# Kernel tuning notes

Measured on AMD Instinct MI355X. Metric: run time of the kernel, lower is better.

Reference implementation:

```python
import jax, jax.numpy as jnp
import numpy as np

D_MODEL = 1024
H = 16
D_K = D_MODEL // H


def setup_inputs() -> dict:
    key = jax.random.key(0)
    ks = jax.random.split(key, 9)
    s = 0.02
    x = jax.random.normal(ks[0], (2, 2048, D_MODEL), dtype=jnp.float32)
    Wq = jax.random.normal(ks[1], (D_MODEL, D_MODEL), dtype=jnp.float32) * s
    bq = jax.random.normal(ks[2], (D_MODEL,), dtype=jnp.float32) * s
    Wk = jax.random.normal(ks[3], (D_MODEL, D_MODEL), dtype=jnp.float32) * s
    bk = jax.random.normal(ks[4], (D_MODEL,), dtype=jnp.float32) * s
    Wv = jax.random.normal(ks[5], (D_MODEL, D_MODEL), dtype=jnp.float32) * s
    bv = jax.random.normal(ks[6], (D_MODEL,), dtype=jnp.float32) * s
    Wo = jax.random.normal(ks[7], (D_MODEL, D_MODEL), dtype=jnp.float32) * s
    bo = jax.random.normal(ks[8], (D_MODEL,), dtype=jnp.float32) * s
    return {"x": x, "Wq": Wq, "bq": bq, "Wk": Wk, "bk": bk,
            "Wv": Wv, "bv": bv, "Wo": Wo, "bo": bo}


def reference(x, Wq, bq, Wk, bk, Wv, bv, Wo, bo):
    b, s, _ = x.shape
    scale = 1.0 / jnp.sqrt(jnp.float32(D_K))
    # projections; [b, s, d] -> [b, h, s, d_k]
    def split_heads(t):
        return t.reshape(b, s, H, D_K).transpose(0, 2, 1, 3)
    q = split_heads(x @ Wq + bq)
    k = split_heads(x @ Wk + bk)
    v = split_heads(x @ Wv + bv)
    scores = jnp.einsum('bhqd,bhkd->bhqk', q, k) * scale  # [b,h,s,s]
    attn = jax.nn.softmax(scores, axis=-1)
    ctx = jnp.einsum('bhqk,bhkd->bhqd', attn, v)
    ctx = ctx.transpose(0, 2, 1, 3).reshape(b, s, D_MODEL)
    return ctx @ Wo + bo + x
```

## Files before the change

kernel.cpp:

```cpp
#include <hip/hip_runtime.h>
#include <hip/hip_bf16.h>
#include <stdint.h>

#define D_MODEL 1024
#define NH 16
#define DK 64
#define S_LEN 2048

typedef __attribute__((ext_vector_type(8))) __bf16 bf16x8;
typedef __attribute__((ext_vector_type(4))) float f32x4;

#define GLOBAL_AS __attribute__((address_space(1)))
#define LDS_AS    __attribute__((address_space(3)))

__device__ __forceinline__ void async16(const ushort* g, ushort* l) {
    __builtin_amdgcn_global_load_lds(
        (const GLOBAL_AS uint32_t*)(uintptr_t)(const void*)g,
        (LDS_AS uint32_t*)(uint32_t)(uintptr_t)(void*)l,
        16, 0, 0);
}

template <int N>
__device__ __forceinline__ void pipe_barrier() {
    asm volatile("s_waitcnt vmcnt(%0)\n\ts_barrier" :: "n"(N) : "memory");
}

__device__ __forceinline__ float fast_exp2(float x) {
    float r;
    asm("v_exp_f32 %0, %1" : "=v"(r) : "v"(x));
    return r;
}

__device__ __forceinline__ ushort f2bf(float f) {
    union { float f; uint32_t u; } v; v.f = f;
    uint32_t lsb = (v.u >> 16) & 1u;
    return (ushort)((v.u + 0x7fffu + lsb) >> 16);
}

__device__ __forceinline__ uint32_t packbf(float a, float b) {
    union { float f; uint32_t u; } x, y; x.f = a; y.f = b;
    return ((x.u + 0x8000u) >> 16) | ((y.u + 0x8000u) & 0xffff0000u);
}

__device__ __forceinline__ bf16x8 ldfrag(const ushort* p) {
    union { uint4 u; bf16x8 b; } cv;
    cv.u = *(const uint4*)p;
    return cv.b;
}


__global__ void cvt_x_kernel(const float* __restrict__ x, ushort* __restrict__ xb) {
    int i = blockIdx.x * 256 + threadIdx.x;
    float4 v = ((const float4*)x)[i];
    ushort4 o;
    o.x = f2bf(v.x); o.y = f2bf(v.y); o.z = f2bf(v.z); o.w = f2bf(v.w);
    ((ushort4*)xb)[i] = o;
}

__global__ void transpose_cvt4_kernel(
    const float* __restrict__ W0, const float* __restrict__ W1,
    const float* __restrict__ W2, const float* __restrict__ W3,
    ushort* __restrict__ D0, ushort* __restrict__ D1,
    ushort* __restrict__ D2, ushort* __restrict__ D3) {
    const float* W; ushort* D;
    switch (blockIdx.z) {
        case 0: W = W0; D = D0; break;
        case 1: W = W1; D = D1; break;
        case 2: W = W2; D = D2; break;
        default: W = W3; D = D3; break;
    }
    __shared__ float tile[32][33];
    int bx = blockIdx.x * 32, by = blockIdx.y * 32;
    int tx = threadIdx.x, ty = threadIdx.y;
#pragma unroll
    for (int j = 0; j < 32; j += 8)
        tile[ty + j][tx] = W[(size_t)(by + ty + j) * D_MODEL + bx + tx];
    __syncthreads();
#pragma unroll
    for (int j = 0; j < 32; j += 8)
        D[(size_t)(bx + ty + j) * D_MODEL + by + tx] = f2bf(tile[tx][ty + j]);
}

__global__ void cvt_bias_kernel(const float* __restrict__ bq, const float* __restrict__ bk,
                                const float* __restrict__ bv, float* __restrict__ out) {
    int i = blockIdx.x * 256 + threadIdx.x;
    float v = (i < 1024) ? bq[i] : (i < 2048 ? bk[i - 1024] : bv[i - 2048]);
    out[i] = v;
}

template <int MODE>
__global__ __launch_bounds__(256) void gemm_kernel(
    const ushort* __restrict__ A, const ushort* __restrict__ Bt,
    const float* __restrict__ bias,
    ushort* __restrict__ outQ, ushort* __restrict__ outK, ushort* __restrict__ outVt,
    const float* __restrict__ xres, float* __restrict__ outF) {
    constexpr int BN = (MODE == 0) ? 128 : 64;
    constexpr int NI = (MODE == 0) ? 4 : 2;
    constexpr int NS = (MODE == 0) ? 4 : 3;
    __shared__ __align__(16) ushort sA[3][128 * 32];
    __shared__ __align__(16) ushort sB[3][BN * 32];
    const int tid = threadIdx.x;
    const int wave = tid >> 6, lane = tid & 63;
    const int lr = lane & 15, lq = lane >> 4;
    const int srow = lane >> 2;
    const int sc = (lane & 3) ^ ((lane >> 4) & 3);

    const int bid = blockIdx.x;
    const int xcd = bid & 7, lb = bid >> 3;
    int bx, by;
    if (MODE == 0) { bx = xcd * 3 + (lb % 3); by = lb / 3; }
    else           { by = xcd * 4 + (lb & 3); bx = lb >> 2; }
    const int blockM = by * 128;
    const int blockN = bx * BN;
    const int waveM = (wave >> 1) * 64;
    const int waveN = (MODE == 0) ? (wave & 1) * 64 : (wave & 1) * 32;

    auto stage = [&](int k0, ushort* a, ushort* b) {
#pragma unroll
        for (int t = 0; t < 2; t++) {
            int row = wave * 32 + t * 16 + srow;
            async16(&A[(size_t)(blockM + row) * D_MODEL + k0 + sc * 8],
                    &a[(wave * 32 + t * 16) * 32]);
        }
        if (MODE == 0) {
#pragma unroll
            for (int t = 0; t < 2; t++) {
                int row = wave * 32 + t * 16 + srow;
                async16(&Bt[(size_t)(blockN + row) * D_MODEL + k0 + sc * 8],
                        &b[(wave * 32 + t * 16) * 32]);
            }
        } else {
            int row = wave * 16 + srow;
            async16(&Bt[(size_t)(blockN + row) * D_MODEL + k0 + sc * 8],
                    &b[wave * 16 * 32]);
        }
    };

    f32x4 acc[4][NI] = {};
    const int swz = (lq ^ ((lr >> 2) & 3)) * 8;

    stage(0, sA[0], sB[0]);
    stage(32, sA[1], sB[1]);
    __syncthreads();

    int cur = 0;
#pragma unroll 4
    for (int k = 0; k < 32; k++) {
        int nx = cur + 2; if (nx >= 3) nx -= 3;
        if (k + 2 < 32) stage((k + 2) * 32, sA[nx], sB[nx]);
        const ushort* a = sA[cur];
        const ushort* b = sB[cur];
        bf16x8 af[4], bfr[NI];
#pragma unroll
        for (int mi = 0; mi < 4; mi++)
            af[mi] = ldfrag(&a[(waveM + mi * 16 + lr) * 32 + swz]);
#pragma unroll
        for (int ni = 0; ni < NI; ni++)
            bfr[ni] = ldfrag(&b[(waveN + ni * 16 + lr) * 32 + swz]);
#pragma unroll
        for (int mi = 0; mi < 4; mi++)
#pragma unroll
            for (int ni = 0; ni < NI; ni++)
                acc[mi][ni] = __builtin_amdgcn_mfma_f32_16x16x32_bf16(
                    af[mi], bfr[ni], acc[mi][ni], 0, 0, 0);
        if (k < 30) pipe_barrier<NS>();
        else if (k == 30) pipe_barrier<0>();
        cur = (cur == 2) ? 0 : cur + 1;
    }

#pragma unroll
    for (int mi = 0; mi < 4; mi++) {
#pragma unroll
        for (int ni = 0; ni < NI; ni++) {
#pragma unroll
            for (int r = 0; r < 4; r++) {
                int m = blockM + waveM + mi * 16 + lq * 4 + r;
                int n = blockN + waveN + ni * 16 + lr;
                float v = acc[mi][ni][r] + bias[n];
                if (MODE == 0) {
                    int which = n >> 10, c = n & 1023;
                    int h = c >> 6, d = c & 63;
                    int b2 = m >> 11, s = m & 2047;
                    size_t bh = (size_t)(b2 * NH + h);
                    if (which == 0)
                        outQ[(bh * S_LEN + s) * DK + d] = f2bf(v * 0.1803368801f);
                    else if (which == 1)
                        outK[(bh * S_LEN + s) * DK + d] = f2bf(v);
                    else
                        outVt[(bh * DK + d) * S_LEN + s] = f2bf(v);
                } else {
                    size_t idx = (size_t)m * D_MODEL + n;
                    outF[idx] = v + xres[idx];
                }
            }
        }
    }
}

__global__ __launch_bounds__(256, 2) void attn_kernel(
    const ushort* __restrict__ Q, const ushort* __restrict__ Km,
    const ushort* __restrict__ Vt, ushort* __restrict__ ctx) {
    const int bid = blockIdx.x;
    const int xcd = bid & 7, lb = bid >> 3;
    const int bh = xcd * 4 + (lb & 3);
    const int qt = lb >> 2;
    const int q0 = qt * 128;
    __shared__ __align__(16) ushort sK[3][64 * 64];
    __shared__ __align__(16) ushort sV[3][64 * 64];
    __shared__ __align__(16) ushort sQP[4][32 * 64];
    const int tid = threadIdx.x;
    const int wave = tid >> 6, lane = tid & 63;
    const int lr = lane & 15, lq = lane >> 4;
    const int srow = lane >> 3, sp = lane & 7;
    const ushort* Qh = Q + (size_t)bh * S_LEN * DK;
    const ushort* Kh = Km + (size_t)bh * S_LEN * DK;
    const ushort* Vh = Vt + (size_t)bh * DK * S_LEN;
    ushort* sPw = sQP[wave];

#pragma unroll
    for (int t = 0; t < 4; t++) {
        int row = t * 8 + srow;
        int c = sp ^ (row & 7);
        async16(&Qh[(size_t)(q0 + wave * 32 + row) * DK + c * 8],
                &sPw[t * 8 * 64]);
    }

    auto stageKV = [&](int k0, int buf) {
#pragma unroll
        for (int t = 0; t < 2; t++) {
            int row = wave * 16 + t * 8 + srow;
            int c = sp ^ (row & 7);
            async16(&Kh[(size_t)(k0 + row) * DK + c * 8],
                    &sK[buf][(wave * 16 + t * 8) * 64]);
            async16(&Vh[(size_t)row * S_LEN + k0 + c * 8],
                    &sV[buf][(wave * 16 + t * 8) * 64]);
        }
    };

    stageKV(0, 0);
    stageKV(64, 1);
    __syncthreads();

    bf16x8 qf[2][2];
#pragma unroll
    for (int nj = 0; nj < 2; nj++)
#pragma unroll
        for (int kk = 0; kk < 2; kk++)
            qf[nj][kk] = ldfrag(&sPw[(nj * 16 + lr) * 64 +
                                     (((kk * 4 + lq) ^ (lr & 7)) * 8)]);

    union { uint4 u; bf16x8 b; } one_u;
    one_u.u = make_uint4(0x3F803F80u, 0x3F803F80u, 0x3F803F80u, 0x3F803F80u);
    const bf16x8 ones = one_u.b;

    f32x4 cacc[2][4] = {};
    f32x4 ssum[2] = {};

    int cur = 0;
    for (int k = 0; k < 32; k++) {
        int nx = cur + 2; if (nx >= 3) nx -= 3;
        if (k + 2 < 32) stageKV((k + 2) * 64, nx);
        const ushort* sk = sK[cur];
        const ushort* sv = sV[cur];

        f32x4 sacc[4][2] = {};
#pragma unroll
        for (int kk = 0; kk < 2; kk++) {
            bf16x8 kf[4];
            int swz = ((kk * 4 + lq) ^ (lr & 7)) * 8;
#pragma unroll
            for (int mi = 0; mi < 4; mi++)
                kf[mi] = ldfrag(&sk[(mi * 16 + lr) * 64 + swz]);
#pragma unroll
            for (int mi = 0; mi < 4; mi++)
#pragma unroll
                for (int nj = 0; nj < 2; nj++)
                    sacc[mi][nj] = __builtin_amdgcn_mfma_f32_16x16x32_bf16(
                        kf[mi], qf[nj][kk], sacc[mi][nj], 0, 0, 0);
        }

#pragma unroll
        for (int mi = 0; mi < 4; mi++)
#pragma unroll
            for (int nj = 0; nj < 2; nj++) {
                float p0 = fast_exp2(sacc[mi][nj][0]);
                float p1 = fast_exp2(sacc[mi][nj][1]);
                float p2 = fast_exp2(sacc[mi][nj][2]);
                float p3 = fast_exp2(sacc[mi][nj][3]);
                uint2 w;
                w.x = packbf(p0, p1);
                w.y = packbf(p2, p3);
                int physc = (mi * 2 + (lq >> 1)) ^ (lr & 7);
                *(uint2*)&sPw[(nj * 16 + lr) * 64 + physc * 8 + (lq & 1) * 4] = w;
            }

#pragma unroll
        for (int ks = 0; ks < 2; ks++) {
            bf16x8 pf[2], vf[4];
            int swz = ((ks * 4 + lq) ^ (lr & 7)) * 8;
#pragma unroll
            for (int nj = 0; nj < 2; nj++)
                pf[nj] = ldfrag(&sPw[(nj * 16 + lr) * 64 + swz]);
#pragma unroll
            for (int nd = 0; nd < 4; nd++)
                vf[nd] = ldfrag(&sv[(nd * 16 + lr) * 64 + swz]);
#pragma unroll
            for (int nj = 0; nj < 2; nj++)
#pragma unroll
                for (int nd = 0; nd < 4; nd++)
                    cacc[nj][nd] = __builtin_amdgcn_mfma_f32_16x16x32_bf16(
                        pf[nj], vf[nd], cacc[nj][nd], 0, 0, 0);
#pragma unroll
            for (int nj = 0; nj < 2; nj++)
                ssum[nj] = __builtin_amdgcn_mfma_f32_16x16x32_bf16(
                    pf[nj], ones, ssum[nj], 0, 0, 0);
        }

        if (k < 30) pipe_barrier<4>();
        else if (k == 30) pipe_barrier<0>();
        cur = (cur == 2) ? 0 : cur + 1;
    }

    const int b = bh >> 4, h = bh & 15;
    float inv[2][4];
#pragma unroll
    for (int nj = 0; nj < 2; nj++)
#pragma unroll
        for (int r = 0; r < 4; r++)
            inv[nj][r] = __builtin_amdgcn_rcpf(ssum[nj][r]);
#pragma unroll
    for (int nj = 0; nj < 2; nj++)
#pragma unroll
        for (int nd = 0; nd < 4; nd++)
#pragma unroll
            for (int r = 0; r < 4; r++) {
                int qrow = q0 + wave * 32 + nj * 16 + lq * 4 + r;
                int d = nd * 16 + lr;
                float v = cacc[nj][nd][r] * inv[nj][r];
                ctx[(size_t)(b * S_LEN + qrow) * D_MODEL + h * DK + d] = f2bf(v);
            }
}


extern "C" void kernel_launch(void* const* d_in, const int* in_sizes, int n_in,
                              void* d_out, int out_size, void* d_ws, size_t ws_size,
                              hipStream_t stream) {
    const float* x  = (const float*)d_in[0];
    const float* Wq = (const float*)d_in[1];
    const float* bq = (const float*)d_in[2];
    const float* Wk = (const float*)d_in[3];
    const float* bk = (const float*)d_in[4];
    const float* Wv = (const float*)d_in[5];
    const float* bv = (const float*)d_in[6];
    const float* Wo = (const float*)d_in[7];
    const float* bo = (const float*)d_in[8];

    char* ws = (char*)d_ws;
    ushort* xb    = (ushort*)(ws);
    ushort* wqkv  = (ushort*)(ws + (8ull  << 20));
    ushort* wo_t  = (ushort*)(ws + (14ull << 20));
    ushort* qbuf  = (ushort*)(ws + (16ull << 20));
    ushort* kbuf  = (ushort*)(ws + (24ull << 20));
    ushort* vtb   = (ushort*)(ws + (32ull << 20));
    ushort* ctx   = (ushort*)(ws + (40ull << 20));
    float*  biasq = (float*)(ws + (48ull << 20));

    cvt_x_kernel<<<4096, 256, 0, stream>>>(x, xb);
    transpose_cvt4_kernel<<<dim3(32, 32, 4), dim3(32, 8), 0, stream>>>(
        Wq, Wk, Wv, Wo, wqkv, wqkv + 1024 * 1024, wqkv + 2 * 1024 * 1024, wo_t);
    cvt_bias_kernel<<<12, 256, 0, stream>>>(bq, bk, bv, biasq);

    gemm_kernel<0><<<768, 256, 0, stream>>>(
        xb, wqkv, biasq, qbuf, kbuf, vtb, nullptr, nullptr);
    attn_kernel<<<512, 256, 0, stream>>>(qbuf, kbuf, vtb, ctx);
    gemm_kernel<1><<<512, 256, 0, stream>>>(
        ctx, wo_t, bo, nullptr, nullptr, nullptr, x, (float*)d_out);
}
```

Baseline: 211.9 us.

## Stage GEMM epilogue through LDS for vectorized stores and deepen pipeline

Replaces the per-element scattered epilogue stores with a pass through shared memory, so Q/K, the transposed V and the fp32 residual output are written as 16-byte coalesced vectors. The K-loop moves from three to four shared-memory stages with a new row-pair XOR swizzle layout for the async global-to-LDS loads, keeping more loads in flight. This adds an extra LDS round trip and barrier in the epilogue, and increases shared memory per block, which may reduce occupancy.

```diff
diff --git a/kernel.cpp b/kernel.cpp
--- a/kernel.cpp
+++ b/kernel.cpp
@@ -97,13 +97,17 @@
     constexpr int BN = (MODE == 0) ? 128 : 64;
     constexpr int NI = (MODE == 0) ? 4 : 2;
     constexpr int NS = (MODE == 0) ? 4 : 3;
-    __shared__ __align__(16) ushort sA[3][128 * 32];
-    __shared__ __align__(16) ushort sB[3][BN * 32];
+    constexpr int ABUF = 4096;
+    constexpr int BBUF = (MODE == 0) ? 4096 : 2048;
+    constexpr int SMEM = (MODE == 0) ? 32768 : 24576;
+    __shared__ __align__(16) ushort smem[SMEM];
+    ushort* sAb = smem;
+    ushort* sBb = smem + 4 * ABUF;
+
     const int tid = threadIdx.x;
     const int wave = tid >> 6, lane = tid & 63;
     const int lr = lane & 15, lq = lane >> 4;
-    const int srow = lane >> 2;
-    const int sc = (lane & 3) ^ ((lane >> 4) & 3);
+    const int srow = lane >> 3, sp = lane & 7;
 
     const int bid = blockIdx.x;
     const int xcd = bid & 7, lb = bid >> 3;
@@ -115,84 +119,156 @@
     const int waveM = (wave >> 1) * 64;
     const int waveN = (MODE == 0) ? (wave & 1) * 64 : (wave & 1) * 32;
 
-    auto stage = [&](int k0, ushort* a, ushort* b) {
+    auto stage = [&](int k0, int buf) {
+        ushort* a = sAb + buf * ABUF;
 #pragma unroll
         for (int t = 0; t < 2; t++) {
-            int row = wave * 32 + t * 16 + srow;
-            async16(&A[(size_t)(blockM + row) * D_MODEL + k0 + sc * 8],
-                    &a[(wave * 32 + t * 16) * 32]);
-        }
+            int Rb = wave * 16 + t * 8;
+            int R = Rb + srow;
+            int L = sp ^ (R & 7);
+            int m = 2 * R + (L >> 2);
+            int kc = L & 3;
+            async16(&A[(size_t)(blockM + m) * D_MODEL + k0 + kc * 8], a + Rb * 64);
+        }
+        ushort* b = sBb + buf * BBUF;
         if (MODE == 0) {
 #pragma unroll
             for (int t = 0; t < 2; t++) {
-                int row = wave * 32 + t * 16 + srow;
-                async16(&Bt[(size_t)(blockN + row) * D_MODEL + k0 + sc * 8],
-                        &b[(wave * 32 + t * 16) * 32]);
+                int Rb = wave * 16 + t * 8;
+                int R = Rb + srow;
+                int L = sp ^ (R & 7);
+                int n = 2 * R + (L >> 2);
+                int kc = L & 3;
+                async16(&Bt[(size_t)(blockN + n) * D_MODEL + k0 + kc * 8], b + Rb * 64);
             }
         } else {
-            int row = wave * 16 + srow;
-            async16(&Bt[(size_t)(blockN + row) * D_MODEL + k0 + sc * 8],
-                    &b[wave * 16 * 32]);
+            int Rb = wave * 8;
+            int R = Rb + srow;
+            int L = sp ^ (R & 7);
+            int n = 2 * R + (L >> 2);
+            int kc = L & 3;
+            async16(&Bt[(size_t)(blockN + n) * D_MODEL + k0 + kc * 8], b + Rb * 64);
         }
     };
 
+    const int RA = (waveM >> 1) + (lr >> 1);
+    const int offA = RA * 64 + ((((lr & 1) * 4 + lq) ^ (RA & 7)) * 8);
+    const int RB = (waveN >> 1) + (lr >> 1);
+    const int offB = RB * 64 + ((((lr & 1) * 4 + lq) ^ (RB & 7)) * 8);
+
     f32x4 acc[4][NI] = {};
-    const int swz = (lq ^ ((lr >> 2) & 3)) * 8;
-
-    stage(0, sA[0], sB[0]);
-    stage(32, sA[1], sB[1]);
-    __syncthreads();
-
-    int cur = 0;
+
+    stage(0, 0);
+    stage(32, 1);
+    stage(64, 2);
+    pipe_barrier<2 * NS>();
+
 #pragma unroll 4
     for (int k = 0; k < 32; k++) {
-        int nx = cur + 2; if (nx >= 3) nx -= 3;
-        if (k + 2 < 32) stage((k + 2) * 32, sA[nx], sB[nx]);
-        const ushort* a = sA[cur];
-        const ushort* b = sB[cur];
+        const int buf = k & 3;
+        if (k + 3 < 32) stage((k + 3) * 32, (k + 3) & 3);
+        const ushort* a = sAb + buf * ABUF;
+        const ushort* b = sBb + buf * BBUF;
         bf16x8 af[4], bfr[NI];
 #pragma unroll
         for (int mi = 0; mi < 4; mi++)
-            af[mi] = ldfrag(&a[(waveM + mi * 16 + lr) * 32 + swz]);
+            af[mi] = ldfrag(&a[offA + mi * 512]);
 #pragma unroll
         for (int ni = 0; ni < NI; ni++)
-            bfr[ni] = ldfrag(&b[(waveN + ni * 16 + lr) * 32 + swz]);
+            bfr[ni] = ldfrag(&b[offB + ni * 512]);
 #pragma unroll
         for (int mi = 0; mi < 4; mi++)
 #pragma unroll
             for (int ni = 0; ni < NI; ni++)
                 acc[mi][ni] = __builtin_amdgcn_mfma_f32_16x16x32_bf16(
                     af[mi], bfr[ni], acc[mi][ni], 0, 0, 0);
-        if (k < 30) pipe_barrier<NS>();
+        if (k < 30) pipe_barrier<2 * NS>();
         else if (k == 30) pipe_barrier<0>();
-        cur = (cur == 2) ? 0 : cur + 1;
     }
-
-#pragma unroll
-    for (int mi = 0; mi < 4; mi++) {
-#pragma unroll
-        for (int ni = 0; ni < NI; ni++) {
-#pragma unroll
-            for (int r = 0; r < 4; r++) {
-                int m = blockM + waveM + mi * 16 + lq * 4 + r;
-                int n = blockN + waveN + ni * 16 + lr;
-                float v = acc[mi][ni][r] + bias[n];
-                if (MODE == 0) {
-                    int which = n >> 10, c = n & 1023;
-                    int h = c >> 6, d = c & 63;
-                    int b2 = m >> 11, s = m & 2047;
-                    size_t bh = (size_t)(b2 * NH + h);
-                    if (which == 0)
-                        outQ[(bh * S_LEN + s) * DK + d] = f2bf(v * 0.1803368801f);
-                    else if (which == 1)
-                        outK[(bh * S_LEN + s) * DK + d] = f2bf(v);
-                    else
-                        outVt[(bh * DK + d) * S_LEN + s] = f2bf(v);
-                } else {
-                    size_t idx = (size_t)m * D_MODEL + n;
-                    outF[idx] = v + xres[idx];
+    __syncthreads();
+
+    const int bglob = blockM >> 11;
+    const int sbase = blockM & 2047;
+
+    if (MODE == 0) {
+        const int which = bx >> 3;
+        if (which < 2) {
+            const float scale = (which == 0) ? 0.1803368801f : 1.0f;
+#pragma unroll
+            for (int ni = 0; ni < 4; ni++) {
+                const int n_loc = waveN + ni * 16 + lr;
+                const float bn = bias[blockN + n_loc];
+#pragma unroll
+                for (int mi = 0; mi < 4; mi++)
+#pragma unroll
+                    for (int r = 0; r < 4; r++) {
+                        int m_loc = waveM + mi * 16 + lq * 4 + r;
+                        smem[m_loc * 136 + n_loc] =
+                            f2bf((acc[mi][ni][r] + bn) * scale);
+                    }
+            }
+            __syncthreads();
+            ushort* outp = (which == 0) ? outQ : outK;
+            const int hbase = (which == 0) ? bx * 2 : (bx - 8) * 2;
+#pragma unroll
+            for (int j = 0; j < 8; j++) {
+                int c = tid + j * 256;
+                int m = c >> 4, nc = c & 15;
+                int hh = nc >> 3, d8 = nc & 7;
+                uint4 w = *(uint4*)&smem[m * 136 + nc * 8];
+                size_t bh = (size_t)(bglob * NH + hbase + hh);
+                *(uint4*)&outp[(bh * S_LEN + sbase + m) * DK + d8 * 8] = w;
+            }
+        } else {
+#pragma unroll
+            for (int ni = 0; ni < 4; ni++) {
+                const int n_loc = waveN + ni * 16 + lr;
+                const float bn = bias[blockN + n_loc];
+#pragma unroll
+                for (int mi = 0; mi < 4; mi++) {
+                    uint2 w;
+                    w.x = packbf(acc[mi][ni][0] + bn, acc[mi][ni][1] + bn);
+                    w.y = packbf(acc[mi][ni][2] + bn, acc[mi][ni][3] + bn);
+                    int m_base = waveM + mi * 16 + lq * 4;
+                    *(uint2*)&smem[n_loc * 136 + m_base] = w;
                 }
             }
+            __syncthreads();
+            const int hbase = (bx - 16) * 2;
+#pragma unroll
+            for (int j = 0; j < 8; j++) {
+                int c = tid + j * 256;
+                int n_loc = c >> 4, m8 = c & 15;
+                int d = n_loc & 63, hh = n_loc >> 6;
+                uint4 w = *(uint4*)&smem[n_loc * 136 + m8 * 8];
+                size_t bh = (size_t)(bglob * NH + hbase + hh);
+                *(uint4*)&outVt[(bh * DK + d) * S_LEN + sbase + m8 * 8] = w;
+            }
+        }
+    } else {
+        float* sCf = (float*)smem;
+#pragma unroll
+        for (int ni = 0; ni < 2; ni++) {
+            const int n_loc = waveN + ni * 16 + lr;
+            const float bn = bias[blockN + n_loc];
+#pragma unroll
+            for (int mi = 0; mi < 4; mi++)
+#pragma unroll
+                for (int r = 0; r < 4; r++) {
+                    int m_loc = waveM + mi * 16 + lq * 4 + r;
+                    sCf[m_loc * 68 + n_loc] = acc[mi][ni][r] + bn;
+                }
+        }
+        __syncthreads();
+#pragma unroll
+        for (int j = 0; j < 8; j++) {
+            int c = tid + j * 256;
+            int m = c >> 4, nc = c & 15;
+            float4 v = *(float4*)&sCf[m * 68 + nc * 4];
+            size_t idx = (size_t)(blockM + m) * D_MODEL + blockN + nc * 4;
+            float4 xr = *(const float4*)&xres[idx];
+            v.x += xr.x; v.y += xr.y; v.z += xr.z; v.w += xr.w;
+            *(float4*)&outF[idx] = v;
         }
     }
 }
```

After: 206.9 us. -2.4%, faster.
